# Kernel optimization log

Measured on AMD Instinct MI355X. Metric: run time of the kernel, lower is better.

Reference implementation:

```python
import jax, jax.numpy as jnp
import numpy as np

B, L, D = 2, 2048, 1024
H, DK, DV = 16, 64, 64
EPS = 1e-6


def setup_inputs() -> dict:
    key = jax.random.key(0)
    ks = jax.random.split(key, 7)
    s = 0.02
    return {
        "x": jax.random.normal(ks[0], (B, L, D), dtype=jnp.float32),
        "Wq": jax.random.normal(ks[1], (D, H * DK), dtype=jnp.float32) * s,
        "Wk": jax.random.normal(ks[2], (D, H * DK), dtype=jnp.float32) * s,
        "Wv": jax.random.normal(ks[3], (D, H * DV), dtype=jnp.float32) * s,
        "Wo": jax.random.normal(ks[4], (H * DV, D), dtype=jnp.float32) * s,
        "ln_gamma": jnp.ones((D,), dtype=jnp.float32),
        "ln_beta": jnp.zeros((D,), dtype=jnp.float32),
    }


def reference(x, Wq, Wk, Wv, Wo, ln_gamma, ln_beta):
    temp = jnp.asarray(DK, x.dtype) ** 0.5
    # projections -> [B, H, L, Dh]
    q = (x @ Wq).reshape(B, L, H, DK).transpose(0, 2, 1, 3)
    k = (x @ Wk).reshape(B, L, H, DK).transpose(0, 2, 1, 3)
    v = (x @ Wv).reshape(B, L, H, DV).transpose(0, 2, 1, 3)
    # naive attention: explicit [B,H,L,L] scores (dropout rate 0 -> identity)
    scores = jnp.einsum("bhqd,bhkd->bhqk", q / temp, k)
    attn = jax.nn.softmax(scores, axis=-1)
    o = jnp.einsum("bhqk,bhkd->bhqd", attn, v)
    o = o.transpose(0, 2, 1, 3).reshape(B, L, H * DV)
    out = o @ Wo + x  # residual
    # LayerNorm(eps=1e-6)
    mu = jnp.mean(out, axis=-1, keepdims=True)
    var = jnp.var(out, axis=-1, keepdims=True)
    return (out - mu) * jax.lax.rsqrt(var + EPS) * ln_gamma + ln_beta
```

## Files before the change

### kernel.cpp

```cpp
#include <hip/hip_runtime.h>


typedef __bf16 bf16;
typedef __bf16 bf16x2 __attribute__((ext_vector_type(2)));
typedef __bf16 bf16x4 __attribute__((ext_vector_type(4)));
typedef __bf16 bf16x8 __attribute__((ext_vector_type(8)));
typedef float floatx4 __attribute__((ext_vector_type(4)));
typedef int intx4 __attribute__((ext_vector_type(4)));

#define MFMA16(a, b, c) __builtin_amdgcn_mfma_f32_16x16x32_bf16((a), (b), (c), 0, 0, 0)

__device__ __forceinline__ void gll16(const bf16* g, bf16* l) {
  __builtin_amdgcn_global_load_lds((const __attribute__((address_space(1))) void*)g,
                                   (__attribute__((address_space(3))) void*)l, 16, 0, 0);
}

__global__ __launch_bounds__(256) void k_prep_x(const float* __restrict__ x, bf16* __restrict__ xb) {
  const int i = (blockIdx.x * 256 + threadIdx.x) * 4;
  const float4 v = *reinterpret_cast<const float4*>(x + i);
  bf16x4 o = {(bf16)v.x, (bf16)v.y, (bf16)v.z, (bf16)v.w};
  *reinterpret_cast<bf16x4*>(xb + i) = o;
}

__global__ __launch_bounds__(256) void k_prep_w(const float* __restrict__ Wq, const float* __restrict__ Wk,
                                                const float* __restrict__ Wv, const float* __restrict__ Wo,
                                                bf16* __restrict__ WT) {
  __shared__ float tile[32][33];
  const int z = blockIdx.z;
  const float* W = (z == 0) ? Wq : (z == 1) ? Wk : (z == 2) ? Wv : Wo;
  const int n0 = blockIdx.x * 32, k0 = blockIdx.y * 32;
  const int tx = threadIdx.x, ty = threadIdx.y;
#pragma unroll
  for (int j = 0; j < 32; j += 8)
    tile[ty + j][tx] = W[(size_t)(k0 + ty + j) * 1024 + n0 + tx];
  __syncthreads();
#pragma unroll
  for (int j = 0; j < 32; j += 8)
    WT[(size_t)(z * 1024 + n0 + ty + j) * 1024 + k0 + tx] = (bf16)tile[tx][ty + j];
}

template <int MODE>
__global__ __launch_bounds__(256) void k_gemm(const bf16* __restrict__ A, const bf16* __restrict__ Bt,
                                              const float* __restrict__ X, float* __restrict__ Y,
                                              bf16* __restrict__ QB, bf16* __restrict__ KB,
                                              bf16* __restrict__ VTB) {
  __shared__ __align__(16) bf16 As[3 * 128 * 64];
  __shared__ __align__(16) bf16 Bs[3 * 128 * 64];
  const int t = threadIdx.x;
  const int lane = t & 63, wv = t >> 6;
  const int qd = lane >> 4, col = lane & 15;
  const int c7 = col & 7;
  const int wm = wv >> 1, wn = wv & 1;
  const int m0 = blockIdx.x * 128, n0 = blockIdx.y * 128;
  const int srow = wv * 8 + (lane >> 3);
  const int scol = ((lane & 7) ^ (lane >> 3)) * 8;
  const bf16* Ag = A + (size_t)(m0 + srow) * 1024 + scol;
  const bf16* Bg = Bt + (size_t)(n0 + srow) * 1024 + scol;

  floatx4 acc[4][4] = {};

#define GSTAGE(bu, ti)                                                                              \
  do {                                                                                              \
    _Pragma("unroll") for (int rd = 0; rd < 4; rd++) {                                              \
      gll16(Ag + (size_t)rd * 32 * 1024 + (ti) * 64, As + (bu) * 8192 + (rd * 32 + wv * 8) * 64);   \
      gll16(Bg + (size_t)rd * 32 * 1024 + (ti) * 64, Bs + (bu) * 8192 + (rd * 32 + wv * 8) * 64);   \
    }                                                                                               \
  } while (0)

#define GCOMP(bu)                                                                                   \
  do {                                                                                              \
    const bf16* as_ = As + (bu) * 8192;                                                             \
    const bf16* bs_ = Bs + (bu) * 8192;                                                             \
    _Pragma("unroll") for (int ks = 0; ks < 2; ks++) {                                              \
      bf16x8 af[4], bfr[4];                                                                         \
      _Pragma("unroll") for (int i = 0; i < 4; i++)                                                 \
        af[i] = *reinterpret_cast<const bf16x8*>(as_ + (wm * 64 + i * 16 + col) * 64 +              \
                                                 ((ks * 4 + qd) ^ c7) * 8);                         \
      _Pragma("unroll") for (int i = 0; i < 4; i++)                                                 \
        bfr[i] = *reinterpret_cast<const bf16x8*>(bs_ + (wn * 64 + i * 16 + col) * 64 +             \
                                                  ((ks * 4 + qd) ^ c7) * 8);                        \
      _Pragma("unroll") for (int i = 0; i < 4; i++)                                                 \
        _Pragma("unroll") for (int j = 0; j < 4; j++)                                               \
          acc[i][j] = MFMA16(af[i], bfr[j], acc[i][j]);                                             \
    }                                                                                               \
  } while (0)

#define GITER(cur, prv, ti)                                            \
  do {                                                                 \
    asm volatile("s_waitcnt vmcnt(8)" ::: "memory");                   \
    __builtin_amdgcn_s_barrier();                                      \
    GCOMP(cur);                                                        \
    __builtin_amdgcn_s_barrier();                                      \
    GSTAGE(prv, ((ti) + 2 <= 15) ? ((ti) + 2) : 15);                   \
  } while (0)

  GSTAGE(0, 0);
  GSTAGE(1, 1);
  asm volatile("s_waitcnt vmcnt(8)" ::: "memory");
  __builtin_amdgcn_s_barrier();
  GCOMP(0);
  __builtin_amdgcn_s_barrier();
  GSTAGE(2, 2);
  for (int j = 1; j < 16; j += 3) {
    GITER(1, 0, j);
    GITER(2, 1, j + 1);
    GITER(0, 2, j + 2);
  }
#undef GSTAGE
#undef GCOMP
#undef GITER

#pragma unroll
  for (int i = 0; i < 4; i++) {
#pragma unroll
    for (int j = 0; j < 4; j++) {
      const int mb = m0 + wm * 64 + i * 16 + qd * 4;
      const int n = n0 + wn * 64 + j * 16 + col;
      if (MODE == 0) {
        const int seg = n >> 10;
        const int h = (n & 1023) >> 6, dd = n & 63;
#pragma unroll
        for (int r = 0; r < 4; r++) {
          const int m = mb + r;
          const int bb = m >> 11, l = m & 2047;
          const float v = acc[i][j][r];
          if (seg == 0)
            QB[((size_t)(bb * 16 + h) * 2048 + l) * 64 + dd] = (bf16)(v * 0.18033688f);
          else if (seg == 1)
            KB[((size_t)(bb * 16 + h) * 2048 + l) * 64 + dd] = (bf16)v;
          else
            VTB[((size_t)(bb * 16 + h) * 64 + dd) * 2048 + l] = (bf16)v;
        }
      } else {
#pragma unroll
        for (int r = 0; r < 4; r++) {
          const int m = mb + r;
          Y[(size_t)m * 1024 + n] = acc[i][j][r] + X[(size_t)m * 1024 + n];
        }
      }
    }
  }
}

__global__ __launch_bounds__(256) void k_attn(const bf16* __restrict__ QB, const bf16* __restrict__ KB,
                                              const bf16* __restrict__ VTB, bf16* __restrict__ OB) {
  __shared__ __align__(16) bf16 Ks[3][64 * 64];
  __shared__ __align__(16) bf16 Vs[3][64 * 64];
  const int t = threadIdx.x;
  const int lane = t & 63, wv = t >> 6;
  const int qd = lane >> 4, col = lane & 15;
  const int c7 = col & 7;
  const int bh = blockIdx.y;
  const int qr = blockIdx.x * 128 + wv * 32;
  const int lrow0 = wv * 8 + (lane >> 3);
  const int scol = ((lane & 7) ^ (lane >> 3)) * 8;
  const int kg0 = ((lrow0 >> 5) << 5) + (((lrow0 >> 2) & 3) << 3) + (((lrow0 >> 4) & 1) << 2) + (lrow0 & 3);
  const int r1 = lrow0 + 32;
  const int kg1 = ((r1 >> 5) << 5) + (((r1 >> 2) & 3) << 3) + (((r1 >> 4) & 1) << 2) + (r1 & 3);
  const bf16* Kg0 = KB + ((size_t)bh * 2048 + kg0) * 64 + scol;
  const bf16* Kg1 = KB + ((size_t)bh * 2048 + kg1) * 64 + scol;
  const bf16* Vg0 = VTB + ((size_t)bh * 64 + lrow0) * 2048 + scol;
  const bf16* Vg1 = VTB + ((size_t)bh * 64 + lrow0 + 32) * 2048 + scol;

  bf16x8 bQ[2][2];
#pragma unroll
  for (int qt = 0; qt < 2; qt++)
#pragma unroll
    for (int s = 0; s < 2; s++)
      bQ[qt][s] = *reinterpret_cast<const bf16x8*>(QB + ((size_t)bh * 2048 + qr + qt * 16 + col) * 64 + s * 32 + qd * 8);

  floatx4 oacc[2][4] = {};
  float lsum[2] = {0.f, 0.f};
  floatx4 scur[2][4];
  int pk[2][4][2];

#define STAGE(bu, ti)                                                  \
  do {                                                                 \
    gll16(Kg0 + (size_t)(ti) * 4096, &Ks[bu][(wv * 8) * 64]);          \
    gll16(Kg1 + (size_t)(ti) * 4096, &Ks[bu][(32 + wv * 8) * 64]);     \
    gll16(Vg0 + (ti) * 64, &Vs[bu][(wv * 8) * 64]);                    \
    gll16(Vg1 + (ti) * 64, &Vs[bu][(32 + wv * 8) * 64]);               \
  } while (0)

#define QK(bu)                                                                                      \
  do {                                                                                              \
    const bf16* ks_ = Ks[bu];                                                                       \
    _Pragma("unroll") for (int nt = 0; nt < 4; nt++) {                                              \
      bf16x8 a0 = *reinterpret_cast<const bf16x8*>(ks_ + (nt * 16 + col) * 64 + (qd ^ c7) * 8);     \
      bf16x8 a1 = *reinterpret_cast<const bf16x8*>(ks_ + (nt * 16 + col) * 64 + ((4 + qd) ^ c7) * 8); \
      _Pragma("unroll") for (int qt = 0; qt < 2; qt++) {                                            \
        floatx4 zz = {0.f, 0.f, 0.f, 0.f};                                                          \
        zz = MFMA16(a0, bQ[qt][0], zz);                                                             \
        zz = MFMA16(a1, bQ[qt][1], zz);                                                             \
        scur[qt][nt] = zz;                                                                          \
      }                                                                                             \
    }                                                                                               \
  } while (0)

#define EXPPACK()                                                                               \
  do {                                                                                          \
    _Pragma("unroll") for (int qt = 0; qt < 2; qt++) {                                          \
      _Pragma("unroll") for (int nt = 0; nt < 4; nt++) {                                        \
        const float e0 = __builtin_amdgcn_exp2f(scur[qt][nt][0]);                               \
        const float e1 = __builtin_amdgcn_exp2f(scur[qt][nt][1]);                               \
        const float e2 = __builtin_amdgcn_exp2f(scur[qt][nt][2]);                               \
        const float e3 = __builtin_amdgcn_exp2f(scur[qt][nt][3]);                               \
        lsum[qt] += (e0 + e1) + (e2 + e3);                                                      \
        bf16x2 p01, p23;                                                                        \
        p01[0] = (bf16)e0; p01[1] = (bf16)e1;                                                   \
        p23[0] = (bf16)e2; p23[1] = (bf16)e3;                                                   \
        pk[qt][nt][0] = __builtin_bit_cast(int, p01);                                           \
        pk[qt][nt][1] = __builtin_bit_cast(int, p23);                                           \
      }                                                                                         \
    }                                                                                           \
  } while (0)

#define PV(bu)                                                                                      \
  do {                                                                                              \
    const bf16* vs_ = Vs[bu];                                                                       \
    bf16x8 bV[4][2];                                                                                \
    _Pragma("unroll") for (int nd = 0; nd < 4; nd++) {                                              \
      bV[nd][0] = *reinterpret_cast<const bf16x8*>(vs_ + (nd * 16 + col) * 64 + (qd ^ c7) * 8);     \
      bV[nd][1] = *reinterpret_cast<const bf16x8*>(vs_ + (nd * 16 + col) * 64 + ((4 + qd) ^ c7) * 8); \
    }                                                                                               \
    _Pragma("unroll") for (int qt = 0; qt < 2; qt++) {                                              \
      _Pragma("unroll") for (int s = 0; s < 2; s++) {                                               \
        intx4 w;                                                                                    \
        w[0] = pk[qt][2 * s][0]; w[1] = pk[qt][2 * s][1];                                           \
        w[2] = pk[qt][2 * s + 1][0]; w[3] = pk[qt][2 * s + 1][1];                                   \
        const bf16x8 aP = __builtin_bit_cast(bf16x8, w);                                            \
        _Pragma("unroll") for (int nd = 0; nd < 4; nd++)                                            \
          oacc[qt][nd] = MFMA16(aP, bV[nd][s], oacc[qt][nd]);                                       \
      }                                                                                             \
    }                                                                                               \
  } while (0)

#define ITER(cur, prv, ti)                                             \
  do {                                                                 \
    asm volatile("s_waitcnt vmcnt(4)" ::: "memory");                   \
    __builtin_amdgcn_s_barrier();                                      \
    EXPPACK();                                                         \
    QK(cur);                                                           \
    PV(prv);                                                           \
    __builtin_amdgcn_s_barrier();                                      \
    STAGE(prv, ((ti) + 2 <= 31) ? ((ti) + 2) : 31);                    \
  } while (0)

  STAGE(0, 0);
  STAGE(1, 1);
  asm volatile("s_waitcnt vmcnt(4)" ::: "memory");
  __builtin_amdgcn_s_barrier();
  QK(0);
  __builtin_amdgcn_s_barrier();
  STAGE(2, 2);
  for (int j = 1; j < 30; j += 3) {
    ITER(1, 0, j);
    ITER(2, 1, j + 1);
    ITER(0, 2, j + 2);
  }
  ITER(1, 0, 31);
  EXPPACK();
  PV(1);

#pragma unroll
  for (int qt = 0; qt < 2; qt++) {
    lsum[qt] += __shfl_xor(lsum[qt], 16);
    lsum[qt] += __shfl_xor(lsum[qt], 32);
  }
  const int bb = bh >> 4, h = bh & 15;
#pragma unroll
  for (int qt = 0; qt < 2; qt++) {
#pragma unroll
    for (int r = 0; r < 4; r++) {
      const float linv = 1.f / __shfl(lsum[qt], qd * 4 + r);
      const size_t m = (size_t)bb * 2048 + qr + qt * 16 + qd * 4 + r;
#pragma unroll
      for (int nd = 0; nd < 4; nd++)
        OB[m * 1024 + h * 64 + nd * 16 + col] = (bf16)(oacc[qt][nd][r] * linv);
    }
  }
#undef STAGE
#undef QK
#undef EXPPACK
#undef PV
#undef ITER
}

__global__ __launch_bounds__(256) void k_ln(const float* __restrict__ Yin, const float* __restrict__ gamma,
                                            const float* __restrict__ beta, float* __restrict__ out) {
  __shared__ float red[8];
  const int row = blockIdx.x, t = threadIdx.x;
  const float4 v = *reinterpret_cast<const float4*>(Yin + (size_t)row * 1024 + t * 4);
  float s = v.x + v.y + v.z + v.w;
  float ss = v.x * v.x + v.y * v.y + v.z * v.z + v.w * v.w;
#pragma unroll
  for (int d = 1; d < 64; d <<= 1) {
    s += __shfl_xor(s, d);
    ss += __shfl_xor(ss, d);
  }
  if ((t & 63) == 0) {
    red[t >> 6] = s;
    red[4 + (t >> 6)] = ss;
  }
  __syncthreads();
  s = red[0] + red[1] + red[2] + red[3];
  ss = red[4] + red[5] + red[6] + red[7];
  const float mu = s * (1.f / 1024.f);
  const float var = ss * (1.f / 1024.f) - mu * mu;
  const float rs = rsqrtf(var + 1e-6f);
  const float4 g = *reinterpret_cast<const float4*>(gamma + t * 4);
  const float4 bt = *reinterpret_cast<const float4*>(beta + t * 4);
  float4 o;
  o.x = (v.x - mu) * rs * g.x + bt.x;
  o.y = (v.y - mu) * rs * g.y + bt.y;
  o.z = (v.z - mu) * rs * g.z + bt.z;
  o.w = (v.w - mu) * rs * g.w + bt.w;
  *reinterpret_cast<float4*>(out + (size_t)row * 1024 + t * 4) = o;
}

extern "C" void kernel_launch(void* const* d_in, const int* in_sizes, int n_in,
                              void* d_out, int out_size, void* d_ws, size_t ws_size,
                              hipStream_t stream) {
  (void)in_sizes; (void)n_in; (void)out_size; (void)ws_size;
  const float* x = (const float*)d_in[0];
  const float* Wq = (const float*)d_in[1];
  const float* Wk = (const float*)d_in[2];
  const float* Wv = (const float*)d_in[3];
  const float* Wo = (const float*)d_in[4];
  const float* gamma = (const float*)d_in[5];
  const float* beta = (const float*)d_in[6];

  char* ws = (char*)d_ws;
  const size_t MB = 1ull << 20;
  bf16* XB = (bf16*)(ws);
  bf16* OB = (bf16*)(ws);
  bf16* WT = (bf16*)(ws + 8 * MB);
  bf16* QB = (bf16*)(ws + 16 * MB);
  bf16* KB = (bf16*)(ws + 24 * MB);
  bf16* VTB = (bf16*)(ws + 32 * MB);
  float* Y = (float*)(ws + 16 * MB);

  k_prep_x<<<4096, 256, 0, stream>>>(x, XB);
  k_prep_w<<<dim3(32, 32, 4), dim3(32, 8), 0, stream>>>(Wq, Wk, Wv, Wo, WT);
  k_gemm<0><<<dim3(32, 24), 256, 0, stream>>>(XB, WT, nullptr, nullptr, QB, KB, VTB);
  k_attn<<<dim3(16, 32), 256, 0, stream>>>(QB, KB, VTB, OB);
  k_gemm<1><<<dim3(32, 8), 256, 0, stream>>>(OB, WT + (size_t)3072 * 1024, x, Y,
                                             nullptr, nullptr, nullptr);
  k_ln<<<4096, 256, 0, stream>>>(Y, gamma, beta, (float*)d_out);
}
```

Baseline: 210.1 us.

## Merge prep kernels, switch GEMM to double buffering, raise attention MFMA priority

Combines the x-cast and weight-transpose kernels into one launch, with the z-grid split between the two jobs, to save a launch. Replaces the GEMM's three-stage LDS pipeline (partial vmcnt waits) with a two-buffer scheme that waits for all loads and syncs after each compute step. This lowers LDS use, which may raise occupancy, but exposes more load latency. Also wraps the attention QK/PV MFMA sections in s_setprio to favor compute waves.

```diff
diff --git a/kernel.cpp b/kernel.cpp
--- a/kernel.cpp
+++ b/kernel.cpp
@@ -15,28 +15,31 @@
                                    (__attribute__((address_space(3))) void*)l, 16, 0, 0);
 }
 
-__global__ __launch_bounds__(256) void k_prep_x(const float* __restrict__ x, bf16* __restrict__ xb) {
-  const int i = (blockIdx.x * 256 + threadIdx.x) * 4;
-  const float4 v = *reinterpret_cast<const float4*>(x + i);
-  bf16x4 o = {(bf16)v.x, (bf16)v.y, (bf16)v.z, (bf16)v.w};
-  *reinterpret_cast<bf16x4*>(xb + i) = o;
-}
-
-__global__ __launch_bounds__(256) void k_prep_w(const float* __restrict__ Wq, const float* __restrict__ Wk,
-                                                const float* __restrict__ Wv, const float* __restrict__ Wo,
-                                                bf16* __restrict__ WT) {
+__global__ __launch_bounds__(256) void k_prep(const float* __restrict__ x,
+                                              const float* __restrict__ Wq, const float* __restrict__ Wk,
+                                              const float* __restrict__ Wv, const float* __restrict__ Wo,
+                                              bf16* __restrict__ xb, bf16* __restrict__ WT) {
   __shared__ float tile[32][33];
   const int z = blockIdx.z;
-  const float* W = (z == 0) ? Wq : (z == 1) ? Wk : (z == 2) ? Wv : Wo;
-  const int n0 = blockIdx.x * 32, k0 = blockIdx.y * 32;
   const int tx = threadIdx.x, ty = threadIdx.y;
-#pragma unroll
-  for (int j = 0; j < 32; j += 8)
-    tile[ty + j][tx] = W[(size_t)(k0 + ty + j) * 1024 + n0 + tx];
-  __syncthreads();
-#pragma unroll
-  for (int j = 0; j < 32; j += 8)
-    WT[(size_t)(z * 1024 + n0 + ty + j) * 1024 + k0 + tx] = (bf16)tile[tx][ty + j];
+  if (z < 4) {
+    const float* W = (z == 0) ? Wq : (z == 1) ? Wk : (z == 2) ? Wv : Wo;
+    const int n0 = blockIdx.x * 32, k0 = blockIdx.y * 32;
+#pragma unroll
+    for (int j = 0; j < 32; j += 8)
+      tile[ty + j][tx] = W[(size_t)(k0 + ty + j) * 1024 + n0 + tx];
+    __syncthreads();
+#pragma unroll
+    for (int j = 0; j < 32; j += 8)
+      WT[(size_t)(z * 1024 + n0 + ty + j) * 1024 + k0 + tx] = (bf16)tile[tx][ty + j];
+  } else {
+    const int blin = blockIdx.y * 32 + blockIdx.x;
+    const int tid = ty * 32 + tx;
+    const size_t i = (((size_t)(z - 4) * 1024 + blin) * 256 + tid) * 4;
+    const float4 v = *reinterpret_cast<const float4*>(x + i);
+    bf16x4 o = {(bf16)v.x, (bf16)v.y, (bf16)v.z, (bf16)v.w};
+    *reinterpret_cast<bf16x4*>(xb + i) = o;
+  }
 }
 
 template <int MODE>
@@ -44,8 +47,8 @@
                                               const float* __restrict__ X, float* __restrict__ Y,
                                               bf16* __restrict__ QB, bf16* __restrict__ KB,
                                               bf16* __restrict__ VTB) {
-  __shared__ __align__(16) bf16 As[3 * 128 * 64];
-  __shared__ __align__(16) bf16 Bs[3 * 128 * 64];
+  __shared__ __align__(16) bf16 As[2 * 128 * 64];
+  __shared__ __align__(16) bf16 Bs[2 * 128 * 64];
   const int t = threadIdx.x;
   const int lane = t & 63, wv = t >> 6;
   const int qd = lane >> 4, col = lane & 15;
@@ -59,18 +62,18 @@
 
   floatx4 acc[4][4] = {};
 
-#define GSTAGE(bu, ti)                                                                              \
+#define GSTAGE(ktv, buf)                                                                            \
   do {                                                                                              \
     _Pragma("unroll") for (int rd = 0; rd < 4; rd++) {                                              \
-      gll16(Ag + (size_t)rd * 32 * 1024 + (ti) * 64, As + (bu) * 8192 + (rd * 32 + wv * 8) * 64);   \
-      gll16(Bg + (size_t)rd * 32 * 1024 + (ti) * 64, Bs + (bu) * 8192 + (rd * 32 + wv * 8) * 64);   \
-    }                                                                                               \
-  } while (0)
-
-#define GCOMP(bu)                                                                                   \
+      gll16(Ag + (size_t)rd * 32 * 1024 + (ktv), As + (buf) * 8192 + (rd * 32 + wv * 8) * 64);      \
+      gll16(Bg + (size_t)rd * 32 * 1024 + (ktv), Bs + (buf) * 8192 + (rd * 32 + wv * 8) * 64);      \
+    }                                                                                               \
+  } while (0)
+
+#define GCOMP(buf)                                                                                  \
   do {                                                                                              \
-    const bf16* as_ = As + (bu) * 8192;                                                             \
-    const bf16* bs_ = Bs + (bu) * 8192;                                                             \
+    const bf16* as_ = As + (buf) * 8192;                                                            \
+    const bf16* bs_ = Bs + (buf) * 8192;                                                            \
     _Pragma("unroll") for (int ks = 0; ks < 2; ks++) {                                              \
       bf16x8 af[4], bfr[4];                                                                         \
       _Pragma("unroll") for (int i = 0; i < 4; i++)                                                 \
@@ -85,30 +88,22 @@
     }                                                                                               \
   } while (0)
 
-#define GITER(cur, prv, ti)                                            \
-  do {                                                                 \
-    asm volatile("s_waitcnt vmcnt(8)" ::: "memory");                   \
-    __builtin_amdgcn_s_barrier();                                      \
-    GCOMP(cur);                                                        \
-    __builtin_amdgcn_s_barrier();                                      \
-    GSTAGE(prv, ((ti) + 2 <= 15) ? ((ti) + 2) : 15);                   \
-  } while (0)
-
   GSTAGE(0, 0);
-  GSTAGE(1, 1);
-  asm volatile("s_waitcnt vmcnt(8)" ::: "memory");
-  __builtin_amdgcn_s_barrier();
-  GCOMP(0);
-  __builtin_amdgcn_s_barrier();
-  GSTAGE(2, 2);
-  for (int j = 1; j < 16; j += 3) {
-    GITER(1, 0, j);
-    GITER(2, 1, j + 1);
-    GITER(0, 2, j + 2);
+  asm volatile("s_waitcnt vmcnt(0)" ::: "memory");
+  __syncthreads();
+
+  for (int kt = 0; kt < 1024; kt += 128) {
+    GSTAGE(kt + 64, 1);
+    GCOMP(0);
+    asm volatile("s_waitcnt vmcnt(0)" ::: "memory");
+    __syncthreads();
+    if (kt + 128 < 1024) GSTAGE(kt + 128, 0);
+    GCOMP(1);
+    asm volatile("s_waitcnt vmcnt(0)" ::: "memory");
+    __syncthreads();
   }
 #undef GSTAGE
 #undef GCOMP
-#undef GITER
 
 #pragma unroll
   for (int i = 0; i < 4; i++) {
@@ -240,8 +235,10 @@
     asm volatile("s_waitcnt vmcnt(4)" ::: "memory");                   \
     __builtin_amdgcn_s_barrier();                                      \
     EXPPACK();                                                         \
+    __builtin_amdgcn_s_setprio(1);                                     \
     QK(cur);                                                           \
     PV(prv);                                                           \
+    __builtin_amdgcn_s_setprio(0);                                     \
     __builtin_amdgcn_s_barrier();                                      \
     STAGE(prv, ((ti) + 2 <= 31) ? ((ti) + 2) : 31);                    \
   } while (0)
@@ -260,7 +257,9 @@
   }
   ITER(1, 0, 31);
   EXPPACK();
+  __builtin_amdgcn_s_setprio(1);
   PV(1);
+  __builtin_amdgcn_s_setprio(0);
 
 #pragma unroll
   for (int qt = 0; qt < 2; qt++) {
@@ -340,8 +339,7 @@
   bf16* VTB = (bf16*)(ws + 32 * MB);
   float* Y = (float*)(ws + 16 * MB);
 
-  k_prep_x<<<4096, 256, 0, stream>>>(x, XB);
-  k_prep_w<<<dim3(32, 32, 4), dim3(32, 8), 0, stream>>>(Wq, Wk, Wv, Wo, WT);
+  k_prep<<<dim3(32, 32, 8), dim3(32, 8), 0, stream>>>(x, Wq, Wk, Wv, Wo, XB, WT);
   k_gemm<0><<<dim3(32, 24), 256, 0, stream>>>(XB, WT, nullptr, nullptr, QB, KB, VTB);
   k_attn<<<dim3(16, 32), 256, 0, stream>>>(QB, KB, VTB, OB);
   k_gemm<1><<<dim3(32, 8), 256, 0, stream>>>(OB, WT + (size_t)3072 * 1024, x, Y,
```

New measurement: 205.2 us. -2.3%, faster.
